# Optimization experiments

Hardware: AMD Instinct MI355X
Metric: run time of the kernel (lower is better)

Reference implementation:

```python
import jax, jax.numpy as jnp
from jax import lax
import numpy as np

H = 64  # hiddenSize
I = 9   # inputSize

def _init_lstm_params(key, in_dim, hidden):
    k = 1.0 / np.sqrt(hidden)
    ks = jax.random.split(key, 4)
    w_ih = jax.random.uniform(ks[0], (4 * hidden, in_dim), minval=-k, maxval=k, dtype=jnp.float32)
    w_hh = jax.random.uniform(ks[1], (4 * hidden, hidden), minval=-k, maxval=k, dtype=jnp.float32)
    b_ih = jax.random.uniform(ks[2], (4 * hidden,), minval=-k, maxval=k, dtype=jnp.float32)
    b_hh = jax.random.uniform(ks[3], (4 * hidden,), minval=-k, maxval=k, dtype=jnp.float32)
    return w_ih, w_hh, b_ih, b_hh

def setup_inputs() -> dict:
    key = jax.random.key(0)
    kx, k0, k1, kl = jax.random.split(key, 4)
    x = jax.random.normal(kx, (4096, 336, I), dtype=jnp.float32)
    w_ih0, w_hh0, b_ih0, b_hh0 = _init_lstm_params(k0, I, H)
    w_ih1, w_hh1, b_ih1, b_hh1 = _init_lstm_params(k1, H, H)
    klw, klb = jax.random.split(kl)
    k = 1.0 / np.sqrt(H)
    w_lin = jax.random.uniform(klw, (1, H), minval=-k, maxval=k, dtype=jnp.float32)
    b_lin = jax.random.uniform(klb, (1,), minval=-k, maxval=k, dtype=jnp.float32)
    return {"x": x, "w_ih0": w_ih0, "w_hh0": w_hh0, "b_ih0": b_ih0, "b_hh0": b_hh0,
            "w_ih1": w_ih1, "w_hh1": w_hh1, "b_ih1": b_ih1, "b_hh1": b_hh1,
            "w_lin": w_lin, "b_lin": b_lin}

def _lstm_layer(x_seq, w_ih, w_hh, b_ih, b_hh):
    # x_seq: [B, T, D] -> hidden sequence [B, T, H]. PyTorch gate order: i, f, g, o.
    B = x_seq.shape[0]
    hidden = w_hh.shape[1]
    # Precompute input contribution for all timesteps in one GEMM.
    pre = jnp.einsum('btd,gd->btg', x_seq, w_ih) + b_ih + b_hh  # [B, T, 4H]
    pre_t = jnp.swapaxes(pre, 0, 1)  # [T, B, 4H]

    def step(carry, p):
        h, c = carry
        gates = p + h @ w_hh.T  # [B, 4H]
        i, f, g, o = jnp.split(gates, 4, axis=-1)
        i = jax.nn.sigmoid(i)
        f = jax.nn.sigmoid(f)
        g = jnp.tanh(g)
        o = jax.nn.sigmoid(o)
        c = f * c + i * g
        h = o * jnp.tanh(c)
        return (h, c), h

    h0 = jnp.zeros((B, hidden), dtype=x_seq.dtype)
    c0 = jnp.zeros((B, hidden), dtype=x_seq.dtype)
    _, hs = lax.scan(step, (h0, c0), pre_t)
    return jnp.swapaxes(hs, 0, 1)  # [B, T, H]

def reference(x, w_ih0, w_hh0, b_ih0, b_hh0, w_ih1, w_hh1, b_ih1, b_hh1, w_lin, b_lin):
    h1 = _lstm_layer(x, w_ih0, w_hh0, b_ih0, b_hh0)     # layer 1 (dropout inactive in eval)
    h2 = _lstm_layer(h1, w_ih1, w_hh1, b_ih1, b_hh1)    # layer 2
    last = h2[:, -1, :]                                  # [B, H]
    out = jax.nn.sigmoid(last @ w_lin.T + b_lin)         # [B, 1]
    return out
```

## Files before the change

### kernel.cpp

```cpp
#include <hip/hip_runtime.h>
#include <hip/hip_bf16.h>
#include <stdint.h>


typedef __attribute__((ext_vector_type(8))) short s16x8;
typedef __attribute__((ext_vector_type(4))) short s16x4;
typedef __attribute__((ext_vector_type(4))) float f32x4;

#define MFMA_BF16 __builtin_amdgcn_mfma_f32_16x16x32_bf16

__device__ __forceinline__ short f2bf(float f) {
    uint32_t u = __builtin_bit_cast(uint32_t, f);
    u += 0x7fffu + ((u >> 16) & 1u);
    return (short)(u >> 16);
}

__device__ __forceinline__ float fsigm(float x) {
    float e = __builtin_amdgcn_exp2f(x * -1.4426950408889634f);
    return __builtin_amdgcn_rcpf(1.0f + e);
}
__device__ __forceinline__ float ftanh(float x) {
    float e = __builtin_amdgcn_exp2f(x * 2.8853900817779268f);
    return 1.0f - 2.0f * __builtin_amdgcn_rcpf(1.0f + e);
}

__global__ __launch_bounds__(512, 1)
void lstm_fused(const float* __restrict__ x,
                const float* __restrict__ w_ih0, const float* __restrict__ w_hh0,
                const float* __restrict__ b_ih0, const float* __restrict__ b_hh0,
                const float* __restrict__ w_ih1, const float* __restrict__ w_hh1,
                const float* __restrict__ b_ih1, const float* __restrict__ b_hh1,
                const float* __restrict__ w_lin, const float* __restrict__ b_lin,
                float* __restrict__ out)
{
    __shared__ __align__(16) short xs[16 * 512];
    __shared__ __align__(16) short h0s[16 * 64];
    __shared__ __align__(16) short h1s[16 * 64];
    __shared__ float red[4][16];

    const int tid  = threadIdx.x;
    const int w    = tid >> 6;
    const int role = w >> 2;
    const int wl   = w & 3;
    const int l    = tid & 63;
    const int bcol = l & 15;
    const int q    = l >> 4;
    const int b0   = blockIdx.x * 16;

    for (int i = tid; i < 16 * 512; i += 512) xs[i] = 0;
    for (int i = tid; i < 16 * 64; i += 512) { h0s[i] = 0; h1s[i] = 0; }
    __syncthreads();

    s16x8 aW[4][4];
    f32x4 bias[4];
    #pragma unroll
    for (int m = 0; m < 4; ++m) {
        const int R = m * 64 + wl * 16 + bcol;
        if (role == 0) {
            #pragma unroll
            for (int r = 0; r < 8; ++r) {
                int k = q * 8 + r;
                aW[m][0][r] = (k < 9) ? f2bf(w_ih0[R * 9 + k]) : (short)0;
            }
            #pragma unroll
            for (int kf = 0; kf < 2; ++kf) {
                const float* p = w_hh0 + R * 64 + kf * 32 + q * 8;
                #pragma unroll
                for (int r = 0; r < 8; ++r) aW[m][1 + kf][r] = f2bf(p[r]);
            }
            #pragma unroll
            for (int r = 0; r < 8; ++r) aW[m][3][r] = 0;
            #pragma unroll
            for (int r = 0; r < 4; ++r) {
                int G = m * 64 + wl * 16 + q * 4 + r;
                bias[m][r] = b_ih0[G] + b_hh0[G];
            }
        } else {
            #pragma unroll
            for (int kf = 0; kf < 4; ++kf) {
                int ks = kf * 32 + q * 8;
                const float* p = (ks < 64) ? (w_ih1 + R * 64 + ks)
                                           : (w_hh1 + R * 64 + (ks - 64));
                #pragma unroll
                for (int r = 0; r < 8; ++r) aW[m][kf][r] = f2bf(p[r]);
            }
            #pragma unroll
            for (int r = 0; r < 4; ++r) {
                int G = m * 64 + wl * 16 + q * 4 + r;
                bias[m][r] = b_ih1[G] + b_hh1[G];
            }
        }
    }

    f32x4 c = {0.f, 0.f, 0.f, 0.f};
    f32x4 hq = {0.f, 0.f, 0.f, 0.f};

    const int hrd0 = bcol * 64 + (((q    ) ^ (bcol & 7)) << 3);
    const int hrd1 = bcol * 64 + (((4 + q) ^ (bcol & 7)) << 3);
    const int hwr  = bcol * 64 + (((wl * 2 + (q >> 1)) ^ (bcol & 7)) << 3)
                   + ((q & 1) << 2);
    const int xrd  = bcol * 32 + ((q ^ (bcol & 3)) << 3);

    const int    ld_b = (tid & 255) >> 4, ld_t = tid & 15;
    const float* xrow = x + (size_t)(b0 + ld_b) * (336 * 9) + ld_t * 9;
    const int    xs_wr_base = ld_t * 512 + ld_b * 32;
    const int    xswzw = (ld_b & 3) << 3;

    #pragma unroll 1
    for (int i = 0; i <= 336; ++i) {
        if ((i & 15) == 0 && i < 336) {
            if (tid < 256) {
                const float* xp = xrow + (size_t)i * 9;
                #pragma unroll
                for (int d = 0; d < 9; ++d)
                    xs[(xs_wr_base + d) ^ xswzw] = f2bf(xp[d]);
            }
            __syncthreads();
        }

        const bool act0 = (role == 0) & (i < 336);
        const bool act1 = (role == 1) & (i > 0);

        s16x4 pv;
        bool wrote = false;
        if (act0) {
            s16x8 bx  = *(const s16x8*)&xs[(i & 15) * 512 + xrd];
            s16x8 ba  = *(const s16x8*)&h0s[hrd0];
            s16x8 bb  = *(const s16x8*)&h0s[hrd1];
            f32x4 acc[4];
            #pragma unroll
            for (int m = 0; m < 4; ++m) acc[m] = MFMA_BF16(aW[m][0], bx, bias[m], 0, 0, 0);
            #pragma unroll
            for (int m = 0; m < 4; ++m) acc[m] = MFMA_BF16(aW[m][1], ba, acc[m], 0, 0, 0);
            #pragma unroll
            for (int m = 0; m < 4; ++m) acc[m] = MFMA_BF16(aW[m][2], bb, acc[m], 0, 0, 0);
            #pragma unroll
            for (int r = 0; r < 4; ++r) {
                float iv = fsigm(acc[0][r]);
                float fv = fsigm(acc[1][r]);
                float gv = ftanh(acc[2][r]);
                float ov = fsigm(acc[3][r]);
                float cc = fv * c[r] + iv * gv;
                c[r] = cc;
                hq[r] = ov * ftanh(cc);
            }
            pv = (s16x4){ f2bf(hq[0]), f2bf(hq[1]), f2bf(hq[2]), f2bf(hq[3]) };
            wrote = true;
        } else if (act1) {
            s16x8 ba  = *(const s16x8*)&h0s[hrd0];
            s16x8 bb  = *(const s16x8*)&h0s[hrd1];
            s16x8 b1a = *(const s16x8*)&h1s[hrd0];
            s16x8 b1b = *(const s16x8*)&h1s[hrd1];
            f32x4 acc[4];
            #pragma unroll
            for (int m = 0; m < 4; ++m) acc[m] = MFMA_BF16(aW[m][0], ba,  bias[m], 0, 0, 0);
            #pragma unroll
            for (int m = 0; m < 4; ++m) acc[m] = MFMA_BF16(aW[m][1], bb,  acc[m], 0, 0, 0);
            #pragma unroll
            for (int m = 0; m < 4; ++m) acc[m] = MFMA_BF16(aW[m][2], b1a, acc[m], 0, 0, 0);
            #pragma unroll
            for (int m = 0; m < 4; ++m) acc[m] = MFMA_BF16(aW[m][3], b1b, acc[m], 0, 0, 0);
            #pragma unroll
            for (int r = 0; r < 4; ++r) {
                float iv = fsigm(acc[0][r]);
                float fv = fsigm(acc[1][r]);
                float gv = ftanh(acc[2][r]);
                float ov = fsigm(acc[3][r]);
                float cc = fv * c[r] + iv * gv;
                c[r] = cc;
                hq[r] = ov * ftanh(cc);
            }
            pv = (s16x4){ f2bf(hq[0]), f2bf(hq[1]), f2bf(hq[2]), f2bf(hq[3]) };
            wrote = true;
        }

        __syncthreads();
        if (wrote) {
            if (role == 0) *(s16x4*)&h0s[hwr] = pv;
            else           *(s16x4*)&h1s[hwr] = pv;
        }
        __syncthreads();
    }

    if (role == 1) {
        float part = hq[0] * w_lin[wl * 16 + q * 4 + 0]
                   + hq[1] * w_lin[wl * 16 + q * 4 + 1]
                   + hq[2] * w_lin[wl * 16 + q * 4 + 2]
                   + hq[3] * w_lin[wl * 16 + q * 4 + 3];
        part += __shfl_xor(part, 16, 64);
        part += __shfl_xor(part, 32, 64);
        if (q == 0) red[wl][bcol] = part;
    }
    __syncthreads();
    if (tid < 16) {
        float s = red[0][tid] + red[1][tid] + red[2][tid] + red[3][tid] + b_lin[0];
        out[b0 + tid] = fsigm(s);
    }
}

extern "C" void kernel_launch(void* const* d_in, const int* in_sizes, int n_in,
                              void* d_out, int out_size, void* d_ws, size_t ws_size,
                              hipStream_t stream) {
    const float* x     = (const float*)d_in[0];
    const float* w_ih0 = (const float*)d_in[1];
    const float* w_hh0 = (const float*)d_in[2];
    const float* b_ih0 = (const float*)d_in[3];
    const float* b_hh0 = (const float*)d_in[4];
    const float* w_ih1 = (const float*)d_in[5];
    const float* w_hh1 = (const float*)d_in[6];
    const float* b_ih1 = (const float*)d_in[7];
    const float* b_hh1 = (const float*)d_in[8];
    const float* w_lin = (const float*)d_in[9];
    const float* b_lin = (const float*)d_in[10];

    lstm_fused<<<dim3(256), dim3(512), 0, stream>>>(
        x, w_ih0, w_hh0, b_ih0, b_hh0,
        w_ih1, w_hh1, b_ih1, b_hh1,
        w_lin, b_lin, (float*)d_out);
}
```

Baseline: 306.4 us.

## Double-buffer LSTM hidden states in LDS to drop one barrier per step

Hidden-state buffers for both layers become ping-pong pairs indexed by timestep parity. Each step reads the previous step's buffer and writes the current one directly, so the barrier that separated reads from writes is removed and only one __syncthreads per step remains. The f32-to-bf16 packing now uses the hardware v_cvt_pk_bf16_f32 instruction in place of the manual rounding sequence. LDS use grows slightly, and the inline asm ties the kernel to targets that support that instruction.

```diff
diff --git a/kernel.cpp b/kernel.cpp
--- a/kernel.cpp
+++ b/kernel.cpp
@@ -13,6 +13,13 @@
     uint32_t u = __builtin_bit_cast(uint32_t, f);
     u += 0x7fffu + ((u >> 16) & 1u);
     return (short)(u >> 16);
+}
+
+__device__ __forceinline__ s16x4 pack_bf16x4(float a, float b, float c, float d) {
+    union { uint32_t u[2]; s16x4 s; } r;
+    asm("v_cvt_pk_bf16_f32 %0, %1, %2" : "=v"(r.u[0]) : "v"(a), "v"(b));
+    asm("v_cvt_pk_bf16_f32 %0, %1, %2" : "=v"(r.u[1]) : "v"(c), "v"(d));
+    return r.s;
 }
 
 __device__ __forceinline__ float fsigm(float x) {
@@ -34,8 +41,8 @@
                 float* __restrict__ out)
 {
     __shared__ __align__(16) short xs[16 * 512];
-    __shared__ __align__(16) short h0s[16 * 64];
-    __shared__ __align__(16) short h1s[16 * 64];
+    __shared__ __align__(16) short h0s[2][16 * 64];
+    __shared__ __align__(16) short h1s[2][16 * 64];
     __shared__ float red[4][16];
 
     const int tid  = threadIdx.x;
@@ -48,7 +55,9 @@
     const int b0   = blockIdx.x * 16;
 
     for (int i = tid; i < 16 * 512; i += 512) xs[i] = 0;
-    for (int i = tid; i < 16 * 64; i += 512) { h0s[i] = 0; h1s[i] = 0; }
+    for (int i = tid; i < 16 * 64; i += 512) {
+        h0s[0][i] = 0; h0s[1][i] = 0; h1s[0][i] = 0; h1s[1][i] = 0;
+    }
     __syncthreads();
 
     s16x8 aW[4][4];
@@ -118,15 +127,18 @@
             __syncthreads();
         }
 
+        const short* h0r = h0s[(i & 1) ^ 1];
+        const short* h1r = h1s[(i & 1) ^ 1];
+        short*       h0w = h0s[i & 1];
+        short*       h1w = h1s[i & 1];
+
         const bool act0 = (role == 0) & (i < 336);
         const bool act1 = (role == 1) & (i > 0);
 
-        s16x4 pv;
-        bool wrote = false;
         if (act0) {
-            s16x8 bx  = *(const s16x8*)&xs[(i & 15) * 512 + xrd];
-            s16x8 ba  = *(const s16x8*)&h0s[hrd0];
-            s16x8 bb  = *(const s16x8*)&h0s[hrd1];
+            s16x8 bx = *(const s16x8*)&xs[(i & 15) * 512 + xrd];
+            s16x8 ba = *(const s16x8*)&h0r[hrd0];
+            s16x8 bb = *(const s16x8*)&h0r[hrd1];
             f32x4 acc[4];
             #pragma unroll
             for (int m = 0; m < 4; ++m) acc[m] = MFMA_BF16(aW[m][0], bx, bias[m], 0, 0, 0);
@@ -144,13 +156,12 @@
                 c[r] = cc;
                 hq[r] = ov * ftanh(cc);
             }
-            pv = (s16x4){ f2bf(hq[0]), f2bf(hq[1]), f2bf(hq[2]), f2bf(hq[3]) };
-            wrote = true;
+            *(s16x4*)&h0w[hwr] = pack_bf16x4(hq[0], hq[1], hq[2], hq[3]);
         } else if (act1) {
-            s16x8 ba  = *(const s16x8*)&h0s[hrd0];
-            s16x8 bb  = *(const s16x8*)&h0s[hrd1];
-            s16x8 b1a = *(const s16x8*)&h1s[hrd0];
-            s16x8 b1b = *(const s16x8*)&h1s[hrd1];
+            s16x8 ba  = *(const s16x8*)&h0r[hrd0];
+            s16x8 bb  = *(const s16x8*)&h0r[hrd1];
+            s16x8 b1a = *(const s16x8*)&h1r[hrd0];
+            s16x8 b1b = *(const s16x8*)&h1r[hrd1];
             f32x4 acc[4];
             #pragma unroll
             for (int m = 0; m < 4; ++m) acc[m] = MFMA_BF16(aW[m][0], ba,  bias[m], 0, 0, 0);
@@ -170,15 +181,9 @@
                 c[r] = cc;
                 hq[r] = ov * ftanh(cc);
             }
-            pv = (s16x4){ f2bf(hq[0]), f2bf(hq[1]), f2bf(hq[2]), f2bf(hq[3]) };
-            wrote = true;
+            *(s16x4*)&h1w[hwr] = pack_bf16x4(hq[0], hq[1], hq[2], hq[3]);
         }
 
-        __syncthreads();
-        if (wrote) {
-            if (role == 0) *(s16x4*)&h0s[hwr] = pv;
-            else           *(s16x4*)&h1s[hwr] = pv;
-        }
         __syncthreads();
     }
 
```

After: 306.1 us. No clear change (-0.1%).

## Replace block barriers with LDS counter spin-waits and ring-buffered hidden state

Applied to the files above, without the earlier changes.

Removes the two __syncthreads per timestep. Layer-0 and layer-1 waves now run decoupled loops that signal progress through per-wave LDS counters, and layer 0 writes its hidden state into an 8-deep ring buffer so it can run several steps ahead of layer 1. The gate scale factors (log2e terms) are folded into the weights and biases, and the nonlinearities share reciprocals across gates, with packed bf16 conversion. This adds spin-wait overhead and memory-ordering risk, and clamped exponent inputs slightly change numerics at the extremes.

```diff
diff --git a/kernel.cpp b/kernel.cpp
--- a/kernel.cpp
+++ b/kernel.cpp
@@ -4,24 +4,68 @@
 
 
 typedef __attribute__((ext_vector_type(8))) short s16x8;
-typedef __attribute__((ext_vector_type(4))) short s16x4;
 typedef __attribute__((ext_vector_type(4))) float f32x4;
 
 #define MFMA_BF16 __builtin_amdgcn_mfma_f32_16x16x32_bf16
-
-__device__ __forceinline__ short f2bf(float f) {
+#define LOG2E     1.4426950408889634f
+#define TWO_LOG2E 2.8853900817779268f
+#define DEPTH     8
+
+static __device__ __forceinline__ short f2bf(float f) {
     uint32_t u = __builtin_bit_cast(uint32_t, f);
     u += 0x7fffu + ((u >> 16) & 1u);
     return (short)(u >> 16);
 }
-
-__device__ __forceinline__ float fsigm(float x) {
-    float e = __builtin_amdgcn_exp2f(x * -1.4426950408889634f);
-    return __builtin_amdgcn_rcpf(1.0f + e);
-}
-__device__ __forceinline__ float ftanh(float x) {
-    float e = __builtin_amdgcn_exp2f(x * 2.8853900817779268f);
-    return 1.0f - 2.0f * __builtin_amdgcn_rcpf(1.0f + e);
+static __device__ __forceinline__ float fexp2(float t){ return __builtin_amdgcn_exp2f(t); }
+static __device__ __forceinline__ float frcp (float t){ return __builtin_amdgcn_rcpf(t); }
+static __device__ __forceinline__ float fclampf(float v, float lo, float hi){
+    return fminf(fmaxf(v, lo), hi);
+}
+
+static __device__ __forceinline__ void spin4(const uint32_t* c, uint32_t need) {
+    const volatile uint32_t* vc = (const volatile uint32_t*)c;
+    for (;;) {
+        uint32_t m0 = vc[0], m1 = vc[1], m2 = vc[2], m3 = vc[3];
+        uint32_t mn = min(min(m0, m1), min(m2, m3));
+        if (mn >= need) break;
+        __builtin_amdgcn_s_sleep(1);
+    }
+    __builtin_amdgcn_sched_barrier(0);
+}
+
+static __device__ __forceinline__ f32x4 nonlin4(const f32x4 acc[4], f32x4& c, uint2& pk) {
+    float ov[4], eg[4];
+    f32x4 h;
+    #pragma unroll
+    for (int r = 0; r < 4; ++r) {
+        float t0 = fclampf(acc[0][r], -30.f, 30.f);
+        float t1 = fclampf(acc[1][r], -30.f, 30.f);
+        float t2 = fclampf(acc[2][r], -30.f, 30.f);
+        float t3 = fclampf(acc[3][r], -30.f, 30.f);
+        float d0 = 1.f + fexp2(t0), d1 = 1.f + fexp2(t1);
+        float d2 = 1.f + fexp2(t2), d3 = 1.f + fexp2(t3);
+        float p01 = d0 * d1, p23 = d2 * d3;
+        float rr  = frcp(p01 * p23);
+        float q01 = rr * p23, q23 = rr * p01;
+        float iv = q01 * d1, fv = q01 * d0;
+        float gv = fmaf(-2.f, q23 * d3, 1.f);
+        ov[r] = q23 * d2;
+        c[r] = fmaf(fv, c[r], iv * gv);
+        eg[r] = fexp2(fclampf(c[r] * TWO_LOG2E, -28.f, 28.f));
+    }
+    {   float dg0 = 1.f + eg[0], dg1 = 1.f + eg[1];
+        float rg = frcp(dg0 * dg1);
+        h[0] = ov[0] * fmaf(-2.f, rg * dg1, 1.f);
+        h[1] = ov[1] * fmaf(-2.f, rg * dg0, 1.f); }
+    {   float dg2 = 1.f + eg[2], dg3 = 1.f + eg[3];
+        float rg = frcp(dg2 * dg3);
+        h[2] = ov[2] * fmaf(-2.f, rg * dg3, 1.f);
+        h[3] = ov[3] * fmaf(-2.f, rg * dg2, 1.f); }
+    uint32_t a_, b_;
+    asm("v_cvt_pk_bf16_f32 %0, %1, %2" : "=v"(a_) : "v"(h[0]), "v"(h[1]));
+    asm("v_cvt_pk_bf16_f32 %0, %1, %2" : "=v"(b_) : "v"(h[2]), "v"(h[3]));
+    pk = make_uint2(a_, b_);
+    return h;
 }
 
 __global__ __launch_bounds__(512, 1)
@@ -33,160 +77,158 @@
                 const float* __restrict__ w_lin, const float* __restrict__ b_lin,
                 float* __restrict__ out)
 {
-    __shared__ __align__(16) short xs[16 * 512];
-    __shared__ __align__(16) short h0s[16 * 64];
-    __shared__ __align__(16) short h1s[16 * 64];
+    __shared__ __align__(16) short    xs[16 * 512];
+    __shared__ __align__(16) uint32_t h0r[DEPTH][512];
+    __shared__ __align__(16) uint32_t h1s[2][512];
+    __shared__ __align__(16) uint32_t cnt[32];
     __shared__ float red[4][16];
 
     const int tid  = threadIdx.x;
     const int w    = tid >> 6;
-    const int role = w >> 2;
-    const int wl   = w & 3;
+    const int role = w & 1;
+    const int wl   = w >> 1;
     const int l    = tid & 63;
     const int bcol = l & 15;
     const int q    = l >> 4;
     const int b0   = blockIdx.x * 16;
 
     for (int i = tid; i < 16 * 512; i += 512) xs[i] = 0;
-    for (int i = tid; i < 16 * 64; i += 512) { h0s[i] = 0; h1s[i] = 0; }
+    if (tid < 512) {
+        #pragma unroll
+        for (int s = 0; s < DEPTH; ++s) h0r[s][tid] = 0;
+        h1s[0][tid] = 0; h1s[1][tid] = 0;
+    }
+    if (tid < 32) cnt[tid] = 0;
     __syncthreads();
 
-    s16x8 aW[4][4];
+    const float scm[4] = { -LOG2E, -LOG2E, TWO_LOG2E, -LOG2E };
+
+    s16x8 aW[16];
     f32x4 bias[4];
     #pragma unroll
     for (int m = 0; m < 4; ++m) {
         const int R = m * 64 + wl * 16 + bcol;
+        const float sc = scm[m];
         if (role == 0) {
             #pragma unroll
             for (int r = 0; r < 8; ++r) {
                 int k = q * 8 + r;
-                aW[m][0][r] = (k < 9) ? f2bf(w_ih0[R * 9 + k]) : (short)0;
-            }
-            #pragma unroll
-            for (int kf = 0; kf < 2; ++kf) {
-                const float* p = w_hh0 + R * 64 + kf * 32 + q * 8;
-                #pragma unroll
-                for (int r = 0; r < 8; ++r) aW[m][1 + kf][r] = f2bf(p[r]);
-            }
-            #pragma unroll
-            for (int r = 0; r < 8; ++r) aW[m][3][r] = 0;
-            #pragma unroll
-            for (int r = 0; r < 4; ++r) {
-                int G = m * 64 + wl * 16 + q * 4 + r;
-                bias[m][r] = b_ih0[G] + b_hh0[G];
+                aW[m][r] = (k < 9) ? f2bf(w_ih0[R * 9 + k] * sc) : (short)0;
+            }
+            const float* pA = w_hh0 + R * 64 + q * 8;
+            const float* pB = w_hh0 + R * 64 + 32 + q * 8;
+            #pragma unroll
+            for (int r = 0; r < 8; ++r) {
+                aW[4 + m][r]  = f2bf(pA[r] * sc);
+                aW[8 + m][r]  = f2bf(pB[r] * sc);
+                aW[12 + m][r] = 0;
             }
         } else {
-            #pragma unroll
-            for (int kf = 0; kf < 4; ++kf) {
-                int ks = kf * 32 + q * 8;
-                const float* p = (ks < 64) ? (w_ih1 + R * 64 + ks)
-                                           : (w_hh1 + R * 64 + (ks - 64));
-                #pragma unroll
-                for (int r = 0; r < 8; ++r) aW[m][kf][r] = f2bf(p[r]);
-            }
-            #pragma unroll
-            for (int r = 0; r < 4; ++r) {
-                int G = m * 64 + wl * 16 + q * 4 + r;
-                bias[m][r] = b_ih1[G] + b_hh1[G];
-            }
-        }
-    }
-
-    f32x4 c = {0.f, 0.f, 0.f, 0.f};
+            const float* pA = w_ih1 + R * 64 + q * 8;
+            const float* pB = w_ih1 + R * 64 + 32 + q * 8;
+            const float* pC = w_hh1 + R * 64 + q * 8;
+            const float* pD = w_hh1 + R * 64 + 32 + q * 8;
+            #pragma unroll
+            for (int r = 0; r < 8; ++r) {
+                aW[m][r]      = f2bf(pA[r] * sc);
+                aW[4 + m][r]  = f2bf(pB[r] * sc);
+                aW[8 + m][r]  = f2bf(pC[r] * sc);
+                aW[12 + m][r] = f2bf(pD[r] * sc);
+            }
+        }
+        const float* bi = (role == 0) ? b_ih0 : b_ih1;
+        const float* bh = (role == 0) ? b_hh0 : b_hh1;
+        #pragma unroll
+        for (int r = 0; r < 4; ++r) {
+            int G = m * 64 + wl * 16 + q * 4 + r;
+            bias[m][r] = (bi[G] + bh[G]) * sc;
+        }
+    }
+
+    const int hswz = (bcol & 7) << 2;
+    const int hk0  = bcol * 32 + ((q * 4) ^ hswz);
+    const int hk1  = bcol * 32 + ((16 + q * 4) ^ hswz);
+    const int hwp  = bcol * 32 + ((wl * 8 + q * 2) ^ hswz);
+    const int xrd  = bcol * 32 + ((q ^ (bcol & 3)) << 3);
+
+    const int    sidx  = wl * 64 + l;
+    const int    ld_b  = sidx >> 4, ld_t = sidx & 15;
+    const float* xrow  = x + (size_t)(b0 + ld_b) * (336 * 9) + ld_t * 9;
+    const int    xs_wr = ld_t * 512 + ld_b * 32;
+    const int    xswzw = (ld_b & 3) << 3;
+
+    uint32_t* const l0c = &cnt[0];
+    uint32_t* const l1c = &cnt[8];
+    uint32_t* const stc = &cnt[16];
+
+    f32x4 c  = {0.f, 0.f, 0.f, 0.f};
     f32x4 hq = {0.f, 0.f, 0.f, 0.f};
-
-    const int hrd0 = bcol * 64 + (((q    ) ^ (bcol & 7)) << 3);
-    const int hrd1 = bcol * 64 + (((4 + q) ^ (bcol & 7)) << 3);
-    const int hwr  = bcol * 64 + (((wl * 2 + (q >> 1)) ^ (bcol & 7)) << 3)
-                   + ((q & 1) << 2);
-    const int xrd  = bcol * 32 + ((q ^ (bcol & 3)) << 3);
-
-    const int    ld_b = (tid & 255) >> 4, ld_t = tid & 15;
-    const float* xrow = x + (size_t)(b0 + ld_b) * (336 * 9) + ld_t * 9;
-    const int    xs_wr_base = ld_t * 512 + ld_b * 32;
-    const int    xswzw = (ld_b & 3) << 3;
-
-    #pragma unroll 1
-    for (int i = 0; i <= 336; ++i) {
-        if ((i & 15) == 0 && i < 336) {
-            if (tid < 256) {
-                const float* xp = xrow + (size_t)i * 9;
+    f32x4 acc[4];
+
+    if (role == 0) {
+        #pragma unroll 1
+        for (int t = 0; t < 336; ++t) {
+            spin4(l0c, t);
+            if ((t & 15) == 0) {
+                const int ck = t >> 4;
+                const float* xp = xrow + (size_t)t * 9;
                 #pragma unroll
                 for (int d = 0; d < 9; ++d)
-                    xs[(xs_wr_base + d) ^ xswzw] = f2bf(xp[d]);
-            }
-            __syncthreads();
-        }
-
-        const bool act0 = (role == 0) & (i < 336);
-        const bool act1 = (role == 1) & (i > 0);
-
-        s16x4 pv;
-        bool wrote = false;
-        if (act0) {
-            s16x8 bx  = *(const s16x8*)&xs[(i & 15) * 512 + xrd];
-            s16x8 ba  = *(const s16x8*)&h0s[hrd0];
-            s16x8 bb  = *(const s16x8*)&h0s[hrd1];
-            f32x4 acc[4];
-            #pragma unroll
-            for (int m = 0; m < 4; ++m) acc[m] = MFMA_BF16(aW[m][0], bx, bias[m], 0, 0, 0);
-            #pragma unroll
-            for (int m = 0; m < 4; ++m) acc[m] = MFMA_BF16(aW[m][1], ba, acc[m], 0, 0, 0);
-            #pragma unroll
-            for (int m = 0; m < 4; ++m) acc[m] = MFMA_BF16(aW[m][2], bb, acc[m], 0, 0, 0);
-            #pragma unroll
-            for (int r = 0; r < 4; ++r) {
-                float iv = fsigm(acc[0][r]);
-                float fv = fsigm(acc[1][r]);
-                float gv = ftanh(acc[2][r]);
-                float ov = fsigm(acc[3][r]);
-                float cc = fv * c[r] + iv * gv;
-                c[r] = cc;
-                hq[r] = ov * ftanh(cc);
-            }
-            pv = (s16x4){ f2bf(hq[0]), f2bf(hq[1]), f2bf(hq[2]), f2bf(hq[3]) };
-            wrote = true;
-        } else if (act1) {
-            s16x8 ba  = *(const s16x8*)&h0s[hrd0];
-            s16x8 bb  = *(const s16x8*)&h0s[hrd1];
-            s16x8 b1a = *(const s16x8*)&h1s[hrd0];
-            s16x8 b1b = *(const s16x8*)&h1s[hrd1];
-            f32x4 acc[4];
-            #pragma unroll
-            for (int m = 0; m < 4; ++m) acc[m] = MFMA_BF16(aW[m][0], ba,  bias[m], 0, 0, 0);
-            #pragma unroll
-            for (int m = 0; m < 4; ++m) acc[m] = MFMA_BF16(aW[m][1], bb,  acc[m], 0, 0, 0);
-            #pragma unroll
-            for (int m = 0; m < 4; ++m) acc[m] = MFMA_BF16(aW[m][2], b1a, acc[m], 0, 0, 0);
-            #pragma unroll
-            for (int m = 0; m < 4; ++m) acc[m] = MFMA_BF16(aW[m][3], b1b, acc[m], 0, 0, 0);
-            #pragma unroll
-            for (int r = 0; r < 4; ++r) {
-                float iv = fsigm(acc[0][r]);
-                float fv = fsigm(acc[1][r]);
-                float gv = ftanh(acc[2][r]);
-                float ov = fsigm(acc[3][r]);
-                float cc = fv * c[r] + iv * gv;
-                c[r] = cc;
-                hq[r] = ov * ftanh(cc);
-            }
-            pv = (s16x4){ f2bf(hq[0]), f2bf(hq[1]), f2bf(hq[2]), f2bf(hq[3]) };
-            wrote = true;
-        }
-
-        __syncthreads();
-        if (wrote) {
-            if (role == 0) *(s16x4*)&h0s[hwr] = pv;
-            else           *(s16x4*)&h1s[hwr] = pv;
-        }
-        __syncthreads();
-    }
+                    xs[(xs_wr + d) ^ xswzw] = f2bf(xp[d]);
+                __threadfence_block();
+                if (l == 0) *(volatile uint32_t*)&stc[wl] = ck + 1;
+                spin4(stc, ck + 1);
+            }
+            s16x8 bx = *(const s16x8*)&xs[(t & 15) * 512 + xrd];
+            const uint32_t* hp = h0r[(t + DEPTH - 1) & (DEPTH - 1)];
+            s16x8 ba = *(const s16x8*)&hp[hk0];
+            s16x8 bb = *(const s16x8*)&hp[hk1];
+            if (t >= DEPTH - 2) spin4(l1c, (uint32_t)(t - (DEPTH - 2)));
+            #pragma unroll
+            for (int m = 0; m < 4; ++m) acc[m] = MFMA_BF16(aW[m],     bx, bias[m], 0, 0, 0);
+            #pragma unroll
+            for (int m = 0; m < 4; ++m) acc[m] = MFMA_BF16(aW[4 + m], ba, acc[m],  0, 0, 0);
+            #pragma unroll
+            for (int m = 0; m < 4; ++m) acc[m] = MFMA_BF16(aW[8 + m], bb, acc[m],  0, 0, 0);
+            uint2 pk;
+            nonlin4(acc, c, pk);
+            *(uint2*)&h0r[t & (DEPTH - 1)][hwp] = pk;
+            __threadfence_block();
+            if (l == 0) *(volatile uint32_t*)&l0c[wl] = t + 1;
+        }
+    } else {
+        #pragma unroll 1
+        for (int t = 0; t < 336; ++t) {
+            spin4(l0c, t + 1);
+            const uint32_t* hp = h0r[t & (DEPTH - 1)];
+            s16x8 ba = *(const s16x8*)&hp[hk0];
+            s16x8 bb = *(const s16x8*)&hp[hk1];
+            spin4(l1c, t);
+            const uint32_t* h1p = h1s[(t + 1) & 1];
+            s16x8 b1a = *(const s16x8*)&h1p[hk0];
+            s16x8 b1b = *(const s16x8*)&h1p[hk1];
+            #pragma unroll
+            for (int m = 0; m < 4; ++m) acc[m] = MFMA_BF16(aW[m],      ba,  bias[m], 0, 0, 0);
+            #pragma unroll
+            for (int m = 0; m < 4; ++m) acc[m] = MFMA_BF16(aW[4 + m],  bb,  acc[m],  0, 0, 0);
+            #pragma unroll
+            for (int m = 0; m < 4; ++m) acc[m] = MFMA_BF16(aW[8 + m],  b1a, acc[m],  0, 0, 0);
+            #pragma unroll
+            for (int m = 0; m < 4; ++m) acc[m] = MFMA_BF16(aW[12 + m], b1b, acc[m],  0, 0, 0);
+            uint2 pk;
+            hq = nonlin4(acc, c, pk);
+            *(uint2*)&h1s[t & 1][hwp] = pk;
+            __threadfence_block();
+            if (l == 0) *(volatile uint32_t*)&l1c[wl] = t + 1;
+        }
+    }
+
+    __syncthreads();
 
     if (role == 1) {
-        float part = hq[0] * w_lin[wl * 16 + q * 4 + 0]
-                   + hq[1] * w_lin[wl * 16 + q * 4 + 1]
-                   + hq[2] * w_lin[wl * 16 + q * 4 + 2]
-                   + hq[3] * w_lin[wl * 16 + q * 4 + 3];
+        const int j0 = wl * 16 + q * 4;
+        float part = hq[0] * w_lin[j0 + 0] + hq[1] * w_lin[j0 + 1]
+                   + hq[2] * w_lin[j0 + 2] + hq[3] * w_lin[j0 + 3];
         part += __shfl_xor(part, 16, 64);
         part += __shfl_xor(part, 32, 64);
         if (q == 0) red[wl][bcol] = part;
@@ -194,7 +236,7 @@
     __syncthreads();
     if (tid < 16) {
         float s = red[0][tid] + red[1][tid] + red[2][tid] + red[3][tid] + b_lin[0];
-        out[b0 + tid] = fsigm(s);
+        out[b0 + tid] = frcp(1.f + fexp2(-s * LOG2E));
     }
 }
 
```

Result: slower. 396.8 us (+29.5%).
